# Kernel optimization log

Hardware: AMD Instinct MI355X
Metric: run time of the kernel (lower is better)

The kernel has to match this reference:

```python
import jax, jax.numpy as jnp
import numpy as np

MARGIN = 40.0


def setup_inputs() -> dict:
    key = jax.random.key(0)
    k1, k2 = jax.random.split(key)
    feat = jax.random.normal(k1, (4096, 512), dtype=jnp.float32)
    targets = jax.random.randint(k2, (4096,), 0, 64, dtype=jnp.int64)
    return {"feat": feat, "targets": targets}


def reference(feat, targets):
    # corr: (n, n) Gram matrix of features
    corr = feat @ feat.T
    # mask[i, j] = True if same class
    mask = targets[:, None] == targets[None, :]
    big = jnp.asarray(jnp.finfo(corr.dtype).max, corr.dtype)
    # per-row min over positives, max over negatives
    corr_ap = jnp.min(jnp.where(mask, corr, big), axis=1)
    corr_an = jnp.max(jnp.where(mask, -big, corr), axis=1)
    # MarginRankingLoss(margin=40) with y = 1: mean(relu(-(ap - an) + margin))
    loss = jnp.mean(jax.nn.relu(corr_an - corr_ap + MARGIN))
    return loss
```

## Files before the change

### kernel.cpp

```cpp
#include <hip/hip_runtime.h>
#include <float.h>
#include <stdint.h>


#define N_ROWS 4096
#define D_K    512
#define BT     128
#define BK     64
#define NKIT   (D_K / BK)
#define NTB    (N_ROWS / BT)
#define NTILES (NTB * (NTB + 1) / 2)
#define MARGIN 40.0f
#define FOLD_BLOCKS 16

typedef __bf16 bf16_t;
typedef bf16_t bf16x8 __attribute__((ext_vector_type(8)));
typedef float  floatx16 __attribute__((ext_vector_type(16)));
typedef unsigned short ushort_t;
typedef ushort_t ushortx8 __attribute__((ext_vector_type(8)));

#define GLOAD_LDS16(g, l)                                        \
    __builtin_amdgcn_global_load_lds(                            \
        (const __attribute__((address_space(1))) void*)(g),      \
        (__attribute__((address_space(3))) void*)(l), 16, 0, 0)

__device__ __forceinline__ ushort_t f2bf_rne(float x) {
    uint32_t u = __builtin_bit_cast(uint32_t, x);
    return (ushort_t)((u + 0x7FFFu + ((u >> 16) & 1u)) >> 16);
}

__global__ __launch_bounds__(256) void cast_kernel(
    const float* __restrict__ f, ushort_t* __restrict__ o,
    int* __restrict__ counter)
{
    const int gid = blockIdx.x * 256 + threadIdx.x;
    if (gid == 0) *counter = 0;

    const int i = gid * 8;
    const float4 v0 = *(const float4*)(f + i);
    const float4 v1 = *(const float4*)(f + i + 4);
    ushortx8 r;
    r[0] = f2bf_rne(v0.x); r[1] = f2bf_rne(v0.y);
    r[2] = f2bf_rne(v0.z); r[3] = f2bf_rne(v0.w);
    r[4] = f2bf_rne(v1.x); r[5] = f2bf_rne(v1.y);
    r[6] = f2bf_rne(v1.z); r[7] = f2bf_rne(v1.w);
    *(ushortx8*)(o + i) = r;
}

__global__ __launch_bounds__(256, 4) void gram_mfma_kernel(
    const ushort_t* __restrict__ fb, const int* __restrict__ tgt,
    float* __restrict__ ap_part, float* __restrict__ an_part)
{
    __shared__ __align__(16) ushort_t As[BT * BK];
    __shared__ __align__(16) ushort_t Bs[BT * BK];
    __shared__ int tgI[BT];
    __shared__ int tgJ[BT];

    float* apRed  = (float*)As;
    float* anRed  = apRed  + 2 * BT;
    float* apRedT = anRed  + 2 * BT;
    float* anRedT = apRedT + 2 * BT;

    int bi = 0, rem = blockIdx.x;
    while (rem >= NTB - bi) { rem -= NTB - bi; ++bi; }
    const int bj = bi + rem;

    const int tid  = threadIdx.x;
    const int i0   = bi * BT;
    const int j0   = bj * BT;
    const int lane = tid & 63;
    const int wave = tid >> 6;
    const int wr   = wave >> 1;
    const int wc   = wave & 1;
    const int cl   = lane & 31;
    const int hh   = lane >> 5;

    if (tid < BT)            tgI[tid]      = tgt[i0 + tid];
    else if (tid < 2 * BT)   tgJ[tid - BT] = tgt[j0 + tid - BT];

    const int sr = tid >> 3;
    const int sc = (tid & 7) ^ (sr & 7);
    const size_t gA0 = (size_t)(i0 + sr) * D_K + sc * 8;
    const size_t gB0 = (size_t)(j0 + sr) * D_K + sc * 8;
    char* AsB = (char*)As;
    char* BsB = (char*)Bs;

    floatx16 acc[2][2];
#pragma unroll
    for (int a = 0; a < 2; ++a)
#pragma unroll
        for (int b = 0; b < 2; ++b) acc[a][b] = (floatx16)0.0f;

    for (int k0 = 0; k0 < D_K; k0 += BK) {
#pragma unroll
        for (int p = 0; p < 4; ++p) {
            GLOAD_LDS16(fb + gA0 + (size_t)p * 32 * D_K + k0,
                        AsB + p * 4096 + tid * 16);
            GLOAD_LDS16(fb + gB0 + (size_t)p * 32 * D_K + k0,
                        BsB + p * 4096 + tid * 16);
        }
        __syncthreads();

#pragma unroll
        for (int s = 0; s < 4; ++s) {
            const int pc8 = ((2 * s + hh) ^ (cl & 7)) * 8;
            bf16x8 a0 = *(const bf16x8*)(As + (wr * 64 + cl) * BK + pc8);
            bf16x8 a1 = *(const bf16x8*)(As + (wr * 64 + 32 + cl) * BK + pc8);
            bf16x8 b0 = *(const bf16x8*)(Bs + (wc * 64 + cl) * BK + pc8);
            bf16x8 b1 = *(const bf16x8*)(Bs + (wc * 64 + 32 + cl) * BK + pc8);
            acc[0][0] = __builtin_amdgcn_mfma_f32_32x32x16_bf16(a0, b0, acc[0][0], 0, 0, 0);
            acc[0][1] = __builtin_amdgcn_mfma_f32_32x32x16_bf16(a0, b1, acc[0][1], 0, 0, 0);
            acc[1][0] = __builtin_amdgcn_mfma_f32_32x32x16_bf16(a1, b0, acc[1][0], 0, 0, 0);
            acc[1][1] = __builtin_amdgcn_mfma_f32_32x32x16_bf16(a1, b1, acc[1][1], 0, 0, 0);
        }
        __syncthreads();
    }

    const int tj0 = tgJ[wc * 64 + cl];
    const int tj1 = tgJ[wc * 64 + 32 + cl];

    float apT[2], anT[2];
#pragma unroll
    for (int cg = 0; cg < 2; ++cg) { apT[cg] = FLT_MAX; anT[cg] = -FLT_MAX; }

#pragma unroll
    for (int rg = 0; rg < 2; ++rg) {
        const int rbase = wr * 64 + rg * 32 + 4 * hh;
#pragma unroll
        for (int reg = 0; reg < 16; ++reg) {
            const int row = rbase + (reg & 3) + 8 * (reg >> 2);
            const int ti = tgI[row];
            const float v0 = acc[rg][0][reg];
            const float v1 = acc[rg][1][reg];
            float vap = FLT_MAX, van = -FLT_MAX;
            if (ti == tj0) { vap = fminf(vap, v0); apT[0] = fminf(apT[0], v0); }
            else           { van = fmaxf(van, v0); anT[0] = fmaxf(anT[0], v0); }
            if (ti == tj1) { vap = fminf(vap, v1); apT[1] = fminf(apT[1], v1); }
            else           { van = fmaxf(van, v1); anT[1] = fmaxf(anT[1], v1); }
#pragma unroll
            for (int m = 1; m < 32; m <<= 1) {
                vap = fminf(vap, __shfl_xor(vap, m));
                van = fmaxf(van, __shfl_xor(van, m));
            }
            if (cl == 0) {
                apRed[wc * BT + row] = vap;
                anRed[wc * BT + row] = van;
            }
        }
    }
#pragma unroll
    for (int cg = 0; cg < 2; ++cg) {
        float vap = apT[cg], van = anT[cg];
        vap = fminf(vap, __shfl_xor(vap, 32));
        van = fmaxf(van, __shfl_xor(van, 32));
        if (lane < 32) {
            apRedT[wr * BT + wc * 64 + cg * 32 + cl] = vap;
            anRedT[wr * BT + wc * 64 + cg * 32 + cl] = van;
        }
    }
    __syncthreads();

    if (tid < BT) {
        ap_part[(size_t)bj * N_ROWS + i0 + tid] =
            fminf(apRed[0 * BT + tid], apRed[1 * BT + tid]);
        an_part[(size_t)bj * N_ROWS + i0 + tid] =
            fmaxf(anRed[0 * BT + tid], anRed[1 * BT + tid]);
        if (bi != bj) {
            ap_part[(size_t)bi * N_ROWS + j0 + tid] =
                fminf(apRedT[0 * BT + tid], apRedT[1 * BT + tid]);
            an_part[(size_t)bi * N_ROWS + j0 + tid] =
                fmaxf(anRedT[0 * BT + tid], anRedT[1 * BT + tid]);
        }
    }
}

__global__ __launch_bounds__(256) void fold_kernel(
    const float* __restrict__ ap_part, const float* __restrict__ an_part,
    float* __restrict__ blk_sum, int* __restrict__ counter,
    float* __restrict__ out)
{
    __shared__ float sred[4];
    const int tid = threadIdx.x;
    const int row = blockIdx.x * 256 + tid;
    const int lane = tid & 63;
    const int wave = tid >> 6;

    float ap = FLT_MAX, an = -FLT_MAX;
#pragma unroll 8
    for (int s = 0; s < NTB; ++s) {
        ap = fminf(ap, ap_part[(size_t)s * N_ROWS + row]);
        an = fmaxf(an, an_part[(size_t)s * N_ROWS + row]);
    }
    const float v = an - ap + MARGIN;
    float local = (v > 0.0f) ? v : 0.0f;
#pragma unroll
    for (int m = 32; m >= 1; m >>= 1) local += __shfl_down(local, m);
    if (lane == 0) sred[wave] = local;
    __syncthreads();

    if (tid == 0) {
        blk_sum[blockIdx.x] = sred[0] + sred[1] + sred[2] + sred[3];
        __threadfence();
        if (atomicAdd(counter, 1) == FOLD_BLOCKS - 1) {
            __threadfence();
            float s = 0.0f;
#pragma unroll
            for (int b = 0; b < FOLD_BLOCKS; ++b) s += blk_sum[b];
            out[0] = s * (1.0f / N_ROWS);
        }
    }
}

extern "C" void kernel_launch(void* const* d_in, const int* in_sizes, int n_in,
                              void* d_out, int out_size, void* d_ws, size_t ws_size,
                              hipStream_t stream)
{
    const float* feat = (const float*)d_in[0];
    const int*   tgt  = (const int*)d_in[1];

    ushort_t* fb      = (ushort_t*)d_ws;
    float*    ap_part = (float*)(fb + (size_t)N_ROWS * D_K);
    float*    an_part = ap_part + (size_t)NTB * N_ROWS;
    float*    blk_sum = an_part + (size_t)NTB * N_ROWS;
    int*      counter = (int*)(blk_sum + FOLD_BLOCKS);

    cast_kernel<<<(N_ROWS * D_K) / (256 * 8), 256, 0, stream>>>(feat, fb, counter);
    gram_mfma_kernel<<<NTILES, 256, 0, stream>>>(fb, tgt, ap_part, an_part);
    fold_kernel<<<FOLD_BLOCKS, 256, 0, stream>>>(ap_part, an_part, blk_sum,
                                                 counter, (float*)d_out);
}
```

Before: 90.64 us.

## Pre-pack bf16 features in MFMA fragment order and load operands directly from global

The cast kernel now stages 32-row slabs in LDS and writes the bf16 features in a layout that matches the MFMA 32x32x16 operand fragments, so each lane's 8-element chunk is contiguous. The Gram kernel drops LDS staging and the per-k-step barriers, and instead streams fragments straight from global memory with a one-step register prefetch. This removes LDS traffic and sync overhead, but every wave now reads its operands from global or L2 with no sharing across waves inside a block, which doubles global read traffic per block and depends on cache hits and latency hiding.

Result: no change. 92.28 us (+1.8%).

```diff
diff --git a/kernel.cpp b/kernel.cpp
--- a/kernel.cpp
+++ b/kernel.cpp
@@ -6,23 +6,18 @@
 #define N_ROWS 4096
 #define D_K    512
 #define BT     128
-#define BK     64
-#define NKIT   (D_K / BK)
+#define NKB    (D_K / 16)
 #define NTB    (N_ROWS / BT)
 #define NTILES (NTB * (NTB + 1) / 2)
 #define MARGIN 40.0f
 #define FOLD_BLOCKS 16
+#define RBLK   (32 * 64 * 8)
 
 typedef __bf16 bf16_t;
 typedef bf16_t bf16x8 __attribute__((ext_vector_type(8)));
+typedef bf16_t bf16x4 __attribute__((ext_vector_type(4)));
 typedef float  floatx16 __attribute__((ext_vector_type(16)));
 typedef unsigned short ushort_t;
-typedef ushort_t ushortx8 __attribute__((ext_vector_type(8)));
-
-#define GLOAD_LDS16(g, l)                                        \
-    __builtin_amdgcn_global_load_lds(                            \
-        (const __attribute__((address_space(1))) void*)(g),      \
-        (__attribute__((address_space(3))) void*)(l), 16, 0, 0)
 
 __device__ __forceinline__ ushort_t f2bf_rne(float x) {
     uint32_t u = __builtin_bit_cast(uint32_t, x);
@@ -30,36 +25,57 @@
 }
 
 __global__ __launch_bounds__(256) void cast_kernel(
-    const float* __restrict__ f, ushort_t* __restrict__ o,
+    const float* __restrict__ f, ushort_t* __restrict__ fbp,
     int* __restrict__ counter)
 {
-    const int gid = blockIdx.x * 256 + threadIdx.x;
-    if (gid == 0) *counter = 0;
-
-    const int i = gid * 8;
-    const float4 v0 = *(const float4*)(f + i);
-    const float4 v1 = *(const float4*)(f + i + 4);
-    ushortx8 r;
-    r[0] = f2bf_rne(v0.x); r[1] = f2bf_rne(v0.y);
-    r[2] = f2bf_rne(v0.z); r[3] = f2bf_rne(v0.w);
-    r[4] = f2bf_rne(v1.x); r[5] = f2bf_rne(v1.y);
-    r[6] = f2bf_rne(v1.z); r[7] = f2bf_rne(v1.w);
-    *(ushortx8*)(o + i) = r;
-}
+    __shared__ __align__(16) ushort_t lds[32 * 512];
+    const int R   = blockIdx.x;
+    const int tid = threadIdx.x;
+    if (R == 0 && tid == 0) *counter = 0;
+
+#pragma unroll
+    for (int p = 0; p < 16; ++p) {
+        const int fi   = p * 256 + tid;
+        const int row  = fi >> 7;
+        const int col4 = fi & 127;
+        const float4 v = *(const float4*)(f + ((size_t)(R * 32 + row) << 9) + col4 * 4);
+        bf16x4 o;
+        o[0] = __builtin_bit_cast(bf16_t, f2bf_rne(v.x));
+        o[1] = __builtin_bit_cast(bf16_t, f2bf_rne(v.y));
+        o[2] = __builtin_bit_cast(bf16_t, f2bf_rne(v.z));
+        o[3] = __builtin_bit_cast(bf16_t, f2bf_rne(v.w));
+        const int chunk = (col4 >> 1) ^ (row & 7);
+        *(bf16x4*)(lds + row * 512 + chunk * 8 + (col4 & 1) * 4) = o;
+    }
+    __syncthreads();
+
+#pragma unroll
+    for (int p = 0; p < 8; ++p) {
+        const int c  = p * 256 + tid;
+        const int l  = c & 63;
+        const int r  = l & 31;
+        const int lc = ((c >> 6) * 2 + (l >> 5)) ^ (r & 7);
+        const bf16x8 val = *(const bf16x8*)(lds + r * 512 + lc * 8);
+        *(bf16x8*)(fbp + (size_t)R * RBLK + (size_t)c * 8) = val;
+    }
+}
+
+#define MFMA4()                                                               \
+    do {                                                                      \
+        acc[0][0] = __builtin_amdgcn_mfma_f32_32x32x16_bf16(a0, b0, acc[0][0], 0, 0, 0); \
+        acc[0][1] = __builtin_amdgcn_mfma_f32_32x32x16_bf16(a0, b1, acc[0][1], 0, 0, 0); \
+        acc[1][0] = __builtin_amdgcn_mfma_f32_32x32x16_bf16(a1, b0, acc[1][0], 0, 0, 0); \
+        acc[1][1] = __builtin_amdgcn_mfma_f32_32x32x16_bf16(a1, b1, acc[1][1], 0, 0, 0); \
+    } while (0)
 
 __global__ __launch_bounds__(256, 4) void gram_mfma_kernel(
-    const ushort_t* __restrict__ fb, const int* __restrict__ tgt,
+    const ushort_t* __restrict__ fbp, const int* __restrict__ tgt,
     float* __restrict__ ap_part, float* __restrict__ an_part)
 {
-    __shared__ __align__(16) ushort_t As[BT * BK];
-    __shared__ __align__(16) ushort_t Bs[BT * BK];
     __shared__ int tgI[BT];
     __shared__ int tgJ[BT];
-
-    float* apRed  = (float*)As;
-    float* anRed  = apRed  + 2 * BT;
-    float* apRedT = anRed  + 2 * BT;
-    float* anRedT = apRedT + 2 * BT;
+    __shared__ float apRed[2 * BT], anRed[2 * BT];
+    __shared__ float apRedT[2 * BT], anRedT[2 * BT];
 
     int bi = 0, rem = blockIdx.x;
     while (rem >= NTB - bi) { rem -= NTB - bi; ++bi; }
@@ -75,15 +91,12 @@
     const int cl   = lane & 31;
     const int hh   = lane >> 5;
 
-    if (tid < BT)            tgI[tid]      = tgt[i0 + tid];
-    else if (tid < 2 * BT)   tgJ[tid - BT] = tgt[j0 + tid - BT];
-
-    const int sr = tid >> 3;
-    const int sc = (tid & 7) ^ (sr & 7);
-    const size_t gA0 = (size_t)(i0 + sr) * D_K + sc * 8;
-    const size_t gB0 = (size_t)(j0 + sr) * D_K + sc * 8;
-    char* AsB = (char*)As;
-    char* BsB = (char*)Bs;
+    if (tid < BT) tgI[tid] = tgt[i0 + tid];
+    else          tgJ[tid - BT] = tgt[j0 + tid - BT];
+    __syncthreads();
+
+    const ushort_t* pA = fbp + (size_t)(bi * 4 + wr * 2) * RBLK + lane * 8;
+    const ushort_t* pB = fbp + (size_t)(bj * 4 + wc * 2) * RBLK + lane * 8;
 
     floatx16 acc[2][2];
 #pragma unroll
@@ -91,30 +104,22 @@
 #pragma unroll
         for (int b = 0; b < 2; ++b) acc[a][b] = (floatx16)0.0f;
 
-    for (int k0 = 0; k0 < D_K; k0 += BK) {
-#pragma unroll
-        for (int p = 0; p < 4; ++p) {
-            GLOAD_LDS16(fb + gA0 + (size_t)p * 32 * D_K + k0,
-                        AsB + p * 4096 + tid * 16);
-            GLOAD_LDS16(fb + gB0 + (size_t)p * 32 * D_K + k0,
-                        BsB + p * 4096 + tid * 16);
-        }
-        __syncthreads();
-
-#pragma unroll
-        for (int s = 0; s < 4; ++s) {
-            const int pc8 = ((2 * s + hh) ^ (cl & 7)) * 8;
-            bf16x8 a0 = *(const bf16x8*)(As + (wr * 64 + cl) * BK + pc8);
-            bf16x8 a1 = *(const bf16x8*)(As + (wr * 64 + 32 + cl) * BK + pc8);
-            bf16x8 b0 = *(const bf16x8*)(Bs + (wc * 64 + cl) * BK + pc8);
-            bf16x8 b1 = *(const bf16x8*)(Bs + (wc * 64 + 32 + cl) * BK + pc8);
-            acc[0][0] = __builtin_amdgcn_mfma_f32_32x32x16_bf16(a0, b0, acc[0][0], 0, 0, 0);
-            acc[0][1] = __builtin_amdgcn_mfma_f32_32x32x16_bf16(a0, b1, acc[0][1], 0, 0, 0);
-            acc[1][0] = __builtin_amdgcn_mfma_f32_32x32x16_bf16(a1, b0, acc[1][0], 0, 0, 0);
-            acc[1][1] = __builtin_amdgcn_mfma_f32_32x32x16_bf16(a1, b1, acc[1][1], 0, 0, 0);
-        }
-        __syncthreads();
-    }
+    bf16x8 a0 = *(const bf16x8*)(pA);
+    bf16x8 a1 = *(const bf16x8*)(pA + RBLK);
+    bf16x8 b0 = *(const bf16x8*)(pB);
+    bf16x8 b1 = *(const bf16x8*)(pB + RBLK);
+
+#pragma unroll 4
+    for (int kb = 0; kb < NKB - 1; ++kb) {
+        const int o = (kb + 1) * 512;
+        const bf16x8 na0 = *(const bf16x8*)(pA + o);
+        const bf16x8 na1 = *(const bf16x8*)(pA + RBLK + o);
+        const bf16x8 nb0 = *(const bf16x8*)(pB + o);
+        const bf16x8 nb1 = *(const bf16x8*)(pB + RBLK + o);
+        MFMA4();
+        a0 = na0; a1 = na1; b0 = nb0; b1 = nb1;
+    }
+    MFMA4();
 
     const int tj0 = tgJ[wc * 64 + cl];
     const int tj1 = tgJ[wc * 64 + 32 + cl];
@@ -162,14 +167,14 @@
 
     if (tid < BT) {
         ap_part[(size_t)bj * N_ROWS + i0 + tid] =
-            fminf(apRed[0 * BT + tid], apRed[1 * BT + tid]);
+            fminf(apRed[tid], apRed[BT + tid]);
         an_part[(size_t)bj * N_ROWS + i0 + tid] =
-            fmaxf(anRed[0 * BT + tid], anRed[1 * BT + tid]);
+            fmaxf(anRed[tid], anRed[BT + tid]);
         if (bi != bj) {
             ap_part[(size_t)bi * N_ROWS + j0 + tid] =
-                fminf(apRedT[0 * BT + tid], apRedT[1 * BT + tid]);
+                fminf(apRedT[tid], apRedT[BT + tid]);
             an_part[(size_t)bi * N_ROWS + j0 + tid] =
-                fmaxf(anRedT[0 * BT + tid], anRedT[1 * BT + tid]);
+                fmaxf(anRedT[tid], anRedT[BT + tid]);
         }
     }
 }
@@ -218,14 +223,14 @@
     const float* feat = (const float*)d_in[0];
     const int*   tgt  = (const int*)d_in[1];
 
-    ushort_t* fb      = (ushort_t*)d_ws;
-    float*    ap_part = (float*)(fb + (size_t)N_ROWS * D_K);
+    ushort_t* fbp     = (ushort_t*)d_ws;
+    float*    ap_part = (float*)(fbp + (size_t)N_ROWS * D_K);
     float*    an_part = ap_part + (size_t)NTB * N_ROWS;
     float*    blk_sum = an_part + (size_t)NTB * N_ROWS;
     int*      counter = (int*)(blk_sum + FOLD_BLOCKS);
 
-    cast_kernel<<<(N_ROWS * D_K) / (256 * 8), 256, 0, stream>>>(feat, fb, counter);
-    gram_mfma_kernel<<<NTILES, 256, 0, stream>>>(fb, tgt, ap_part, an_part);
+    cast_kernel<<<N_ROWS / 32, 256, 0, stream>>>(feat, fbp, counter);
+    gram_mfma_kernel<<<NTILES, 256, 0, stream>>>(fbp, tgt, ap_part, an_part);
     fold_kernel<<<FOLD_BLOCKS, 256, 0, stream>>>(ap_part, an_part, blk_sum,
                                                  counter, (float*)d_out);
 }
```
